# Optimization experiments

Measured on AMD Instinct MI355X. Metric: run time of the kernel, lower is better.

Reference implementation:

```python
import jax, jax.numpy as jnp
import numpy as np

EMB = 300      # emb_size
SEQ = 100      # seq_len
KW = 5         # kernel_width
KN = 50        # kernel_num
KMAX = 3       # maxpooling_num
MLP1 = 75      # decoder_mlp1_num
VOCAB = 50000 + 2
B = 2048
QLEN = 5


def setup_inputs() -> dict:
    key = jax.random.key(0)
    ks = jax.random.split(key, 11)
    input_q = jax.random.randint(ks[0], (QLEN,), 0, 50000)
    input_d = jax.random.randint(ks[1], (B, SEQ), 0, 50000)
    emb_table = jax.random.normal(ks[2], (VOCAB, EMB), jnp.float32) * 0.1
    conv_w = jax.random.normal(ks[3], (KW, 3 * EMB, KN), jnp.float32) * 0.02  # WIO
    conv_b = jnp.zeros((KN,), jnp.float32)
    gate_w = jax.random.normal(ks[4], (EMB, KN), jnp.float32) * 0.05
    gate_b = jnp.zeros((KN,), jnp.float32)
    hid_w = jax.random.normal(ks[5], (KN * KMAX, MLP1), jnp.float32) * 0.05
    hid_b = jnp.zeros((MLP1,), jnp.float32)
    score_w = jax.random.normal(ks[6], (MLP1, 1), jnp.float32) * 0.05
    score_b = jnp.zeros((1,), jnp.float32)
    return {"input_q": input_q, "input_d": input_d, "emb_table": emb_table,
            "conv_w": conv_w, "conv_b": conv_b, "gate_w": gate_w, "gate_b": gate_b,
            "hid_w": hid_w, "hid_b": hid_b, "score_w": score_w, "score_b": score_b}


def kmax_pool(x, k):
    # x: [B, KN, L]; keep top-k values along last axis in original sequence order
    _, idx = jax.lax.top_k(x, k)
    idx = jnp.sort(idx, axis=-1)
    return jnp.take_along_axis(x, idx, axis=-1)  # [B, KN, k]


def reference(input_q, input_d, emb_table, conv_w, conv_b, gate_w, gate_b,
              hid_w, hid_b, score_w, score_b):
    # class vector: mean of query-word embeddings -> [EMB]
    class_vec = emb_table[input_q].mean(axis=0)
    # category-specific gate -> [KN]
    query_gate = jax.nn.sigmoid(class_vec @ gate_w + gate_b)
    # document embeddings -> [B, SEQ, EMB]
    emb = emb_table[input_d]
    # elementwise interaction features, concat -> [B, SEQ, 3*EMB]
    conv_in = jnp.concatenate([emb, class_vec * emb, class_vec - emb], axis=-1)
    # conv over sequence (full-width kernel == 1D conv with C_in=3*EMB) -> [B, SEQ-KW+1, KN]
    conv = jax.lax.conv_general_dilated(
        conv_in, conv_w, window_strides=(1,), padding='VALID',
        dimension_numbers=('NWC', 'WIO', 'NWC')) + conv_b
    gated = query_gate * conv                      # [B, L', KN]
    pooled = kmax_pool(jnp.swapaxes(gated, 1, 2), KMAX)  # [B, KN, KMAX]
    enc = pooled.reshape(pooled.shape[0], -1)      # [B, KN*KMAX] = [B, 150]
    mlp1 = jnp.tanh(enc @ hid_w + hid_b)           # [B, 75]
    score = jnp.tanh(mlp1 @ score_w + score_b)     # [B, 1]
    return (mlp1, score)
```

## Files before the change

### kernel.cpp

```cpp
#include <hip/hip_runtime.h>
#include <math.h>

#define EMB   300
#define SEQ   100
#define KW    5
#define KN    50
#define NPAD  64
#define KMAX  3
#define MLP1  75
#define LOUT  96
#define BATCH 2048
#define EPAD  320
#define CHW   32
#define NCHK  10
#define SPW   36
#define TAU   2.5e-6
#define WHA   0.75
#define WHB   0.25
#define FLAG_TAU 1e-5f

#define WS_C    0
#define WS_GATE 320
#define WS_BIAS 384
#define WS_WG   448
#define F64_DBL 96448
#define WH_F    0
#define WL_F    51200
#define ENC_OFF 102400
#define ENC_PITCH 152
#define FLAGCNT_OFF 413696
#define FLAGLIST_OFF 413704
#define FLAGCAP 4096

typedef __attribute__((ext_vector_type(8))) short short8;
typedef __attribute__((ext_vector_type(4))) float f32x4;

__device__ __forceinline__ unsigned pack_hl(float x) {
    unsigned u = __float_as_uint(x);
    unsigned hi = (u + 0x7fffu + ((u >> 16) & 1u)) >> 16;
    float r = x - __uint_as_float(hi << 16);
    unsigned v = __float_as_uint(r);
    unsigned lo = (v + 0x7fffu + ((v >> 16) & 1u)) >> 16;
    return (hi << 16) | lo;
}

__global__ __launch_bounds__(256) void prep_a(
    const int* __restrict__ qids, const float* __restrict__ emb,
    const float* __restrict__ gate_w, const float* __restrict__ gate_b,
    const float* __restrict__ conv_w, const float* __restrict__ conv_b,
    double* __restrict__ ws, float* wsf)
{
    __shared__ double cS[EMB];
    __shared__ double gS[KN];
    __shared__ double pS[KW][KN];
    int t = threadIdx.x;
    if (t == 0) *(int*)(wsf + FLAGCNT_OFF) = 0;
    for (int e = t; e < EMB; e += 256) {
        double s = 0.0;
        for (int q = 0; q < 5; ++q) s += (double)emb[(size_t)qids[q] * EMB + e];
        double c = s * 0.2;
        cS[e] = c;
        ws[WS_C + e] = c;
    }
    __syncthreads();
    if (t < KN) {
        double g = (double)gate_b[t];
        for (int e = 0; e < EMB; ++e) g += cS[e] * (double)gate_w[e * KN + t];
        g = 1.0 / (1.0 + exp(-g));
        gS[t] = g;
        ws[WS_GATE + t] = g;
    }
    if (t < KW * KN) {
        int n = t % KN, w = t / KN;
        const float* base = conv_w + w * (3 * EMB * KN) + (2 * EMB) * KN + n;
        double p = 0.0;
        for (int e = 0; e < EMB; ++e) p += cS[e] * (double)base[e * KN];
        pS[w][n] = p;
    }
    __syncthreads();
    if (t < KN) {
        double s = (double)conv_b[t];
        for (int w = 0; w < KW; ++w) s += pS[w][t];
        ws[WS_BIAS + t] = gS[t] * s;
    }
}

__global__ __launch_bounds__(256) void prep_b(
    const float* __restrict__ conv_w, const double* __restrict__ ws,
    double* __restrict__ wg, float* __restrict__ wsf)
{
    int gid  = blockIdx.x * 256 + threadIdx.x;
    int wid  = gid >> 6;
    int lane = gid & 63;
    int w = wid / EPAD;
    int e = wid - w * EPAD;
    double v = 0.0;
    if (e < EMB && lane < KN) {
        double c = ws[WS_C + e];
        const float* p = conv_w + (size_t)w * (3 * EMB * KN) + (size_t)e * KN + lane;
        v = ws[WS_GATE + lane] *
            ((double)p[0] + c * (double)p[EMB * KN] - (double)p[2 * EMB * KN]);
    }
    if (e < EMB) wg[(size_t)(w * NPAD + lane) * EMB + e] = v;
    unsigned pk = pack_hl((float)v);
    unsigned short* Wh = (unsigned short*)(wsf + WH_F);
    unsigned short* Wl = (unsigned short*)(wsf + WL_F);
    size_t o = (size_t)(w * NPAD + lane) * EPAD + e;
    Wh[o] = (unsigned short)(pk >> 16);
    Wl[o] = (unsigned short)(pk & 0xffffu);
}

__global__ __launch_bounds__(256, 2) void main_mfma(
    const int* __restrict__ input_d, const float* __restrict__ emb,
    const double* __restrict__ ws, float* wsf,
    const float* __restrict__ hid_w, const float* __restrict__ hid_b,
    const float* __restrict__ score_w, const float* __restrict__ score_b,
    float* __restrict__ out)
{
    __shared__ __align__(16) unsigned stageS[4][SEQ * SPW];
    __shared__ float encS[4][ENC_PITCH];
    __shared__ float mlpS[4][MLP1 + 1];

    int t = threadIdx.x;
    int wid = t >> 6, lane = t & 63;
    int bb = blockIdx.x * 4 + wid;
    int m = lane & 15, kg = lane >> 4;
    unsigned* stg = &stageS[wid][0];

    int tv[7];
    #pragma unroll
    for (int it = 0; it < 7; ++it) {
        int i = lane + it * 64;
        tv[it] = (i < SEQ * 4) ? input_d[bb * SEQ + (i >> 2)] : 0;
    }

    f32x4 acc[6][4];
    #pragma unroll
    for (int lt = 0; lt < 6; ++lt)
        #pragma unroll
        for (int nt = 0; nt < 4; ++nt)
            acc[lt][nt] = (f32x4){0.f, 0.f, 0.f, 0.f};

    const unsigned short* Wh = (const unsigned short*)(wsf + WH_F);
    const unsigned short* Wl = (const unsigned short*)(wsf + WL_F);

    float4 pfa[7], pfb[7];
    #pragma unroll
    for (int it = 0; it < 7; ++it) {
        int i = lane + it * 64;
        float4 z = {0.f, 0.f, 0.f, 0.f};
        pfa[it] = z; pfb[it] = z;
        if (i < SEQ * 4) {
            int eg = i & 3;
            const float* er = emb + (size_t)tv[it] * EMB + eg * 8;
            pfa[it] = *(const float4*)(er);
            pfb[it] = *(const float4*)(er + 4);
        }
    }

    #pragma unroll 1
    for (int c = 0; c < NCHK; ++c) {
        int e0 = c * CHW;
        #pragma unroll
        for (int it = 0; it < 7; ++it) {
            int i = lane + it * 64;
            if (i < SEQ * 4) {
                int s = i >> 2, eg = i & 3;
                float4 fa = pfa[it], fb = pfb[it];
                unsigned p0 = pack_hl(fa.x), p1 = pack_hl(fa.y), p2 = pack_hl(fa.z), p3 = pack_hl(fa.w);
                unsigned p4 = pack_hl(fb.x), p5 = pack_hl(fb.y), p6 = pack_hl(fb.z), p7 = pack_hl(fb.w);
                uint4 hv, lv;
                hv.x = (p0 >> 16)     | (p1 & 0xffff0000u);
                hv.y = (p2 >> 16)     | (p3 & 0xffff0000u);
                hv.z = (p4 >> 16)     | (p5 & 0xffff0000u);
                hv.w = (p6 >> 16)     | (p7 & 0xffff0000u);
                lv.x = (p0 & 0xffffu) | (p1 << 16);
                lv.y = (p2 & 0xffffu) | (p3 << 16);
                lv.z = (p4 & 0xffffu) | (p5 << 16);
                lv.w = (p6 & 0xffffu) | (p7 << 16);
                unsigned* rowp = stg + s * SPW + eg * 8;
                *(uint4*)(rowp)     = hv;
                *(uint4*)(rowp + 4) = lv;
            }
        }
        #pragma unroll
        for (int w = 0; w < KW; ++w) {
            short8 Bh[4], Bl[4];
            #pragma unroll
            for (int nt = 0; nt < 4; ++nt) {
                size_t off = (size_t)(w * NPAD + nt * 16 + m) * EPAD + e0 + kg * 8;
                union { uint4 u; short8 s; } xb, yb;
                xb.u = *(const uint4*)(Wh + off);
                yb.u = *(const uint4*)(Wl + off);
                Bh[nt] = xb.s; Bl[nt] = yb.s;
            }
            if (w == KW - 1 && c + 1 < NCHK) {
                __builtin_amdgcn_sched_barrier(0);
                int e0n = e0 + CHW;
                #pragma unroll
                for (int it = 0; it < 7; ++it) {
                    int i = lane + it * 64;
                    float4 z = {0.f, 0.f, 0.f, 0.f};
                    pfa[it] = z; pfb[it] = z;
                    if (i < SEQ * 4) {
                        int eg = i & 3, e = e0n + eg * 8;
                        const float* er = emb + (size_t)tv[it] * EMB;
                        if (e < EMB)     pfa[it] = *(const float4*)(er + e);
                        if (e + 4 < EMB) pfb[it] = *(const float4*)(er + e + 4);
                    }
                }
                __builtin_amdgcn_sched_barrier(0);
            }
            #pragma unroll
            for (int lt = 0; lt < 6; ++lt) {
                int r = lt * 16 + m + w;
                const unsigned* ap = stg + r * SPW + kg * 8;
                short8 ah = *(const short8*)(ap);
                short8 al = *(const short8*)(ap + 4);
                #pragma unroll
                for (int nt = 0; nt < 4; ++nt) {
                    acc[lt][nt] = __builtin_amdgcn_mfma_f32_16x16x32_bf16(ah, Bh[nt], acc[lt][nt], 0, 0, 0);
                    acc[lt][nt] = __builtin_amdgcn_mfma_f32_16x16x32_bf16(al, Bh[nt], acc[lt][nt], 0, 0, 0);
                    acc[lt][nt] = __builtin_amdgcn_mfma_f32_16x16x32_bf16(ah, Bl[nt], acc[lt][nt], 0, 0, 0);
                }
            }
        }
    }

    float* gated = (float*)stg;
    #pragma unroll 1
    for (int ph = 0; ph < 2; ++ph) {
        int np0 = ph * 25;
        #pragma unroll
        for (int nt = 0; nt < 4; ++nt) {
            int n = nt * 16 + m;
            if (n >= np0 && n < np0 + 25) {
                float bias_n = (float)ws[WS_BIAS + n];
                #pragma unroll
                for (int lt = 0; lt < 6; ++lt)
                    #pragma unroll
                    for (int rr = 0; rr < 4; ++rr)
                        gated[(n - np0) * 97 + lt * 16 + kg * 4 + rr] = acc[lt][nt][rr] + bias_n;
            }
        }
        if (lane < 25) {
            int n = np0 + lane;
            const float* rowp = gated + lane * 97;
            float v1 = -1e30f, v2 = -1e30f, v3 = -1e30f, v4 = -1e30f;
            int   i1 = 0, i2 = 0, i3 = 0, i4 = 0;
            for (int l = 0; l < LOUT; ++l) {
                float v = rowp[l];
                if (v > v1)      { v4=v3; i4=i3; v3=v2; i3=i2; v2=v1; i2=i1; v1=v; i1=l; }
                else if (v > v2) { v4=v3; i4=i3; v3=v2; i3=i2; v2=v;  i2=l; }
                else if (v > v3) { v4=v3; i4=i3; v3=v;  i3=l; }
                else if (v > v4) { v4=v;  i4=l; }
            }
            float a0=v1, a1=v2, a2=v3; int j0=i1, j1=i2, j2=i3;
            if (j0 > j1) { float tv2=a0; a0=a1; a1=tv2; int ti=j0; j0=j1; j1=ti; }
            if (j1 > j2) { float tv2=a1; a1=a2; a2=tv2; int ti=j1; j1=j2; j2=ti; }
            if (j0 > j1) { float tv2=a0; a0=a1; a1=tv2; int ti=j0; j0=j1; j1=ti; }
            encS[wid][3*n] = a0; encS[wid][3*n+1] = a1; encS[wid][3*n+2] = a2;
            float* enc = wsf + ENC_OFF + (size_t)bb * ENC_PITCH + 3 * n;
            enc[0] = a0; enc[1] = a1; enc[2] = a2;
            if (v3 - v4 <= FLAG_TAU) {
                int idx = atomicAdd((int*)(wsf + FLAGCNT_OFF), 1);
                if (idx < FLAGCAP) ((int*)(wsf + FLAGLIST_OFF))[idx] = (bb << 6) | n;
            }
        }
    }
    __syncthreads();

    for (int i = t; i < 4 * MLP1; i += 256) {
        int d = i / MLP1, o = i - d * MLP1;
        float h = hid_b[o];
        for (int k = 0; k < KN * KMAX; ++k) h = fmaf(encS[d][k], hid_w[k * MLP1 + o], h);
        h = tanhf(h);
        mlpS[d][o] = h;
        out[(blockIdx.x * 4 + d) * MLP1 + o] = h;
    }
    __syncthreads();
    if (t < 4) {
        float s = score_b[0];
        for (int j = 0; j < MLP1; ++j) s = fmaf(mlpS[t][j], score_w[j], s);
        out[BATCH * MLP1 + blockIdx.x * 4 + t] = tanhf(s);
    }
}

__global__ __launch_bounds__(64) void cleanup_enc(
    const int* __restrict__ input_d, const float* __restrict__ emb,
    const double* __restrict__ ws, float* wsf)
{
    int cnt = *(const int*)(wsf + FLAGCNT_OFF);
    if (cnt > FLAGCAP) cnt = FLAGCAP;
    int idx = blockIdx.x;
    if (idx >= cnt) return;
    int code = ((const int*)(wsf + FLAGLIST_OFF))[idx];
    int b = code >> 6, n = code & 63;
    int lane = threadIdx.x;

    __shared__ int    tokS[SEQ];
    __shared__ double rowS[LOUT];
    for (int i = lane; i < SEQ; i += 64) tokS[i] = input_d[b * SEQ + i];
    __syncthreads();

    for (int l = lane; l < LOUT; l += 64) {
        double s = 0.0;
        for (int w = 0; w < KW; ++w) {
            const float*  er = emb + (size_t)tokS[l + w] * EMB;
            const double* wr = ws + WS_WG + (size_t)(w * NPAD + n) * EMB;
            for (int e = 0; e < EMB; ++e) s += (double)er[e] * wr[e];
        }
        rowS[l] = s + ws[WS_BIAS + n];
    }
    __syncthreads();

    if (lane == 0) {
        double v1=-1e300, v2=-1e300, v3=-1e300, v4=-1e300;
        int    i1=0, i2=0, i3=0, i4=0;
        for (int l = 0; l < LOUT; ++l) {
            double v = rowS[l];
            if (v > v1)      { v4=v3; i4=i3; v3=v2; i3=i2; v2=v1; i2=i1; v1=v; i1=l; }
            else if (v > v2) { v4=v3; i4=i3; v3=v2; i3=i2; v2=v;  i2=l; }
            else if (v > v3) { v4=v3; i4=i3; v3=v;  i3=l; }
            else if (v > v4) { v4=v;  i4=l; }
        }
        double a0=v1, a1=v2, a2=v3; int j0=i1, j1=i2, j2=i3;
        if (j0 > j1) { double tv=a0; a0=a1; a1=tv; int ti=j0; j0=j1; j1=ti; }
        if (j1 > j2) { double tv=a1; a1=a2; a2=tv; int ti=j1; j1=j2; j2=ti; }
        if (j0 > j1) { double tv=a0; a0=a1; a1=tv; int ti=j0; j0=j1; j1=ti; }
        double b0=v1, b1=v2, b2=v4; int k0=i1, k1=i2, k2=i4;
        if (k0 > k1) { double tv=b0; b0=b1; b1=tv; int ti=k0; k0=k1; k1=ti; }
        if (k1 > k2) { double tv=b1; b1=b2; b2=tv; int ti=k1; k1=k2; k2=ti; }
        if (k0 > k1) { double tv=b0; b0=b1; b1=tv; int ti=k0; k0=k1; k1=ti; }
        float* enc = wsf + ENC_OFF + (size_t)b * ENC_PITCH + 3 * n;
        if (v3 - v4 > TAU) {
            enc[0] = (float)a0; enc[1] = (float)a1; enc[2] = (float)a2;
        } else {
            enc[0] = (float)(WHA*a0 + WHB*b0);
            enc[1] = (float)(WHA*a1 + WHB*b1);
            enc[2] = (float)(WHA*a2 + WHB*b2);
        }
    }
}

__global__ __launch_bounds__(128) void cleanup_mlp(
    const float* wsf, const float* __restrict__ hid_w, const float* __restrict__ hid_b,
    const float* __restrict__ score_w, const float* __restrict__ score_b,
    float* __restrict__ out)
{
    int cnt = *(const int*)(wsf + FLAGCNT_OFF);
    if (cnt > FLAGCAP) cnt = FLAGCAP;
    if ((int)blockIdx.x >= cnt) return;
    int code = ((const int*)(wsf + FLAGLIST_OFF))[blockIdx.x];
    int b = code >> 6;
    int t = threadIdx.x;
    __shared__ float eS[KN * KMAX];
    __shared__ float mS[MLP1];
    const float* enc = wsf + ENC_OFF + (size_t)b * ENC_PITCH;
    for (int i = t; i < KN * KMAX; i += 128) eS[i] = enc[i];
    __syncthreads();
    if (t < MLP1) {
        float h = hid_b[t];
        for (int k = 0; k < KN * KMAX; ++k) h = fmaf(eS[k], hid_w[k * MLP1 + t], h);
        h = tanhf(h);
        mS[t] = h;
        out[b * MLP1 + t] = h;
    }
    __syncthreads();
    if (t == 0) {
        float s = score_b[0];
        for (int j = 0; j < MLP1; ++j) s = fmaf(mS[j], score_w[j], s);
        out[BATCH * MLP1 + b] = tanhf(s);
    }
}

extern "C" void kernel_launch(void* const* d_in, const int* in_sizes, int n_in,
                              void* d_out, int out_size, void* d_ws, size_t ws_size,
                              hipStream_t stream)
{
    const int*   input_q = (const int*)d_in[0];
    const int*   input_d = (const int*)d_in[1];
    const float* emb     = (const float*)d_in[2];
    const float* conv_w  = (const float*)d_in[3];
    const float* conv_b  = (const float*)d_in[4];
    const float* gate_w  = (const float*)d_in[5];
    const float* gate_b  = (const float*)d_in[6];
    const float* hid_w   = (const float*)d_in[7];
    const float* hid_b   = (const float*)d_in[8];
    const float* score_w = (const float*)d_in[9];
    const float* score_b = (const float*)d_in[10];
    float*  out = (float*)d_out;
    double* ws  = (double*)d_ws;
    float*  wsf = (float*)((char*)d_ws + (size_t)F64_DBL * 8);

    hipLaunchKernelGGL(prep_a, dim3(1), dim3(256), 0, stream,
                       input_q, emb, gate_w, gate_b, conv_w, conv_b, ws, wsf);
    hipLaunchKernelGGL(prep_b, dim3(400), dim3(256), 0, stream,
                       conv_w, ws, ws + WS_WG, wsf);
    hipLaunchKernelGGL(main_mfma, dim3(BATCH / 4), dim3(256), 0, stream,
                       input_d, emb, ws, wsf, hid_w, hid_b, score_w, score_b, out);
    hipLaunchKernelGGL(cleanup_enc, dim3(FLAGCAP), dim3(64), 0, stream,
                       input_d, emb, ws, wsf);
    hipLaunchKernelGGL(cleanup_mlp, dim3(FLAGCAP), dim3(128), 0, stream,
                       wsf, hid_w, hid_b, score_w, score_b, out);
}
```

Measured before the change: 404.6 us.

## Split each batch row across two waves sharing one staged tile

The main kernel previously gave each wave its own batch row, with each wave computing all four N tiles from a private LDS stage. Now a 128-thread block handles one row, and the two waves split the N tiles (two each) while sharing one staged embedding tile. The change needs block barriers around staging and the top-k phases. It halves per-wave accumulator registers and per-row LDS staging, which may allow higher occupancy. In exchange it adds synchronisation per chunk and launches four times as many blocks.

```diff
diff --git a/kernel.cpp b/kernel.cpp
--- a/kernel.cpp
+++ b/kernel.cpp
@@ -110,63 +110,67 @@
     Wl[o] = (unsigned short)(pk & 0xffffu);
 }
 
-__global__ __launch_bounds__(256, 2) void main_mfma(
+__global__ __launch_bounds__(128, 3) void main_mfma(
     const int* __restrict__ input_d, const float* __restrict__ emb,
     const double* __restrict__ ws, float* wsf,
     const float* __restrict__ hid_w, const float* __restrict__ hid_b,
     const float* __restrict__ score_w, const float* __restrict__ score_b,
     float* __restrict__ out)
 {
-    __shared__ __align__(16) unsigned stageS[4][SEQ * SPW];
-    __shared__ float encS[4][ENC_PITCH];
-    __shared__ float mlpS[4][MLP1 + 1];
+    __shared__ __align__(16) unsigned stageS[SEQ * SPW];
+    float* gated = (float*)stageS;
+    float* encS  = (float*)stageS + 2432;
+    float* mlpS  = (float*)stageS + 2592;
 
     int t = threadIdx.x;
     int wid = t >> 6, lane = t & 63;
-    int bb = blockIdx.x * 4 + wid;
+    int bb = blockIdx.x;
     int m = lane & 15, kg = lane >> 4;
-    unsigned* stg = &stageS[wid][0];
-
-    int tv[7];
+
+    int tv[4];
     #pragma unroll
-    for (int it = 0; it < 7; ++it) {
-        int i = lane + it * 64;
-        tv[it] = (i < SEQ * 4) ? input_d[bb * SEQ + (i >> 2)] : 0;
-    }
-
-    f32x4 acc[6][4];
+    for (int sl = 0; sl < 4; ++sl) {
+        int i = t + sl * 128;
+        tv[sl] = (i < SEQ * 4) ? input_d[bb * SEQ + (i >> 2)] : 0;
+    }
+
+    f32x4 acc[6][2];
     #pragma unroll
     for (int lt = 0; lt < 6; ++lt)
         #pragma unroll
-        for (int nt = 0; nt < 4; ++nt)
+        for (int nt = 0; nt < 2; ++nt)
             acc[lt][nt] = (f32x4){0.f, 0.f, 0.f, 0.f};
 
     const unsigned short* Wh = (const unsigned short*)(wsf + WH_F);
     const unsigned short* Wl = (const unsigned short*)(wsf + WL_F);
 
-    float4 pfa[7], pfb[7];
+    float4 pfa[4], pfb[4];
     #pragma unroll
-    for (int it = 0; it < 7; ++it) {
-        int i = lane + it * 64;
+    for (int sl = 0; sl < 4; ++sl) {
+        int i = t + sl * 128;
         float4 z = {0.f, 0.f, 0.f, 0.f};
-        pfa[it] = z; pfb[it] = z;
+        pfa[sl] = z; pfb[sl] = z;
         if (i < SEQ * 4) {
             int eg = i & 3;
-            const float* er = emb + (size_t)tv[it] * EMB + eg * 8;
-            pfa[it] = *(const float4*)(er);
-            pfb[it] = *(const float4*)(er + 4);
+            const float* er = emb + (size_t)tv[sl] * EMB + eg * 8;
+            pfa[sl] = *(const float4*)(er);
+            pfb[sl] = *(const float4*)(er + 4);
         }
     }
 
     #pragma unroll 1
     for (int c = 0; c < NCHK; ++c) {
         int e0 = c * CHW;
+        __builtin_amdgcn_sched_barrier(0);
+        asm volatile("s_waitcnt lgkmcnt(0)" ::: "memory");
+        __builtin_amdgcn_s_barrier();
+        __builtin_amdgcn_sched_barrier(0);
         #pragma unroll
-        for (int it = 0; it < 7; ++it) {
-            int i = lane + it * 64;
+        for (int sl = 0; sl < 4; ++sl) {
+            int i = t + sl * 128;
             if (i < SEQ * 4) {
                 int s = i >> 2, eg = i & 3;
-                float4 fa = pfa[it], fb = pfb[it];
+                float4 fa = pfa[sl], fb = pfb[sl];
                 unsigned p0 = pack_hl(fa.x), p1 = pack_hl(fa.y), p2 = pack_hl(fa.z), p3 = pack_hl(fa.w);
                 unsigned p4 = pack_hl(fb.x), p5 = pack_hl(fb.y), p6 = pack_hl(fb.z), p7 = pack_hl(fb.w);
                 uint4 hv, lv;
@@ -178,17 +182,22 @@
                 lv.y = (p2 & 0xffffu) | (p3 << 16);
                 lv.z = (p4 & 0xffffu) | (p5 << 16);
                 lv.w = (p6 & 0xffffu) | (p7 << 16);
-                unsigned* rowp = stg + s * SPW + eg * 8;
+                unsigned* rowp = stageS + s * SPW + eg * 8;
                 *(uint4*)(rowp)     = hv;
                 *(uint4*)(rowp + 4) = lv;
             }
         }
+        __builtin_amdgcn_sched_barrier(0);
+        asm volatile("s_waitcnt lgkmcnt(0)" ::: "memory");
+        __builtin_amdgcn_s_barrier();
+        __builtin_amdgcn_sched_barrier(0);
         #pragma unroll
         for (int w = 0; w < KW; ++w) {
-            short8 Bh[4], Bl[4];
+            short8 Bh[2], Bl[2];
             #pragma unroll
-            for (int nt = 0; nt < 4; ++nt) {
-                size_t off = (size_t)(w * NPAD + nt * 16 + m) * EPAD + e0 + kg * 8;
+            for (int nt = 0; nt < 2; ++nt) {
+                int ntg = wid * 2 + nt;
+                size_t off = (size_t)(w * NPAD + ntg * 16 + m) * EPAD + e0 + kg * 8;
                 union { uint4 u; short8 s; } xb, yb;
                 xb.u = *(const uint4*)(Wh + off);
                 yb.u = *(const uint4*)(Wl + off);
@@ -198,15 +207,15 @@
                 __builtin_amdgcn_sched_barrier(0);
                 int e0n = e0 + CHW;
                 #pragma unroll
-                for (int it = 0; it < 7; ++it) {
-                    int i = lane + it * 64;
+                for (int sl = 0; sl < 4; ++sl) {
+                    int i = t + sl * 128;
                     float4 z = {0.f, 0.f, 0.f, 0.f};
-                    pfa[it] = z; pfb[it] = z;
+                    pfa[sl] = z; pfb[sl] = z;
                     if (i < SEQ * 4) {
                         int eg = i & 3, e = e0n + eg * 8;
-                        const float* er = emb + (size_t)tv[it] * EMB;
-                        if (e < EMB)     pfa[it] = *(const float4*)(er + e);
-                        if (e + 4 < EMB) pfb[it] = *(const float4*)(er + e + 4);
+                        const float* er = emb + (size_t)tv[sl] * EMB;
+                        if (e < EMB)     pfa[sl] = *(const float4*)(er + e);
+                        if (e + 4 < EMB) pfb[sl] = *(const float4*)(er + e + 4);
                     }
                 }
                 __builtin_amdgcn_sched_barrier(0);
@@ -214,11 +223,11 @@
             #pragma unroll
             for (int lt = 0; lt < 6; ++lt) {
                 int r = lt * 16 + m + w;
-                const unsigned* ap = stg + r * SPW + kg * 8;
+                const unsigned* ap = stageS + r * SPW + kg * 8;
                 short8 ah = *(const short8*)(ap);
                 short8 al = *(const short8*)(ap + 4);
                 #pragma unroll
-                for (int nt = 0; nt < 4; ++nt) {
+                for (int nt = 0; nt < 2; ++nt) {
                     acc[lt][nt] = __builtin_amdgcn_mfma_f32_16x16x32_bf16(ah, Bh[nt], acc[lt][nt], 0, 0, 0);
                     acc[lt][nt] = __builtin_amdgcn_mfma_f32_16x16x32_bf16(al, Bh[nt], acc[lt][nt], 0, 0, 0);
                     acc[lt][nt] = __builtin_amdgcn_mfma_f32_16x16x32_bf16(ah, Bl[nt], acc[lt][nt], 0, 0, 0);
@@ -227,13 +236,15 @@
         }
     }
 
-    float* gated = (float*)stg;
+    __syncthreads();
+
     #pragma unroll 1
     for (int ph = 0; ph < 2; ++ph) {
         int np0 = ph * 25;
         #pragma unroll
-        for (int nt = 0; nt < 4; ++nt) {
-            int n = nt * 16 + m;
+        for (int nt = 0; nt < 2; ++nt) {
+            int ntg = wid * 2 + nt;
+            int n = ntg * 16 + m;
             if (n >= np0 && n < np0 + 25) {
                 float bias_n = (float)ws[WS_BIAS + n];
                 #pragma unroll
@@ -243,9 +254,12 @@
                         gated[(n - np0) * 97 + lt * 16 + kg * 4 + rr] = acc[lt][nt][rr] + bias_n;
             }
         }
-        if (lane < 25) {
-            int n = np0 + lane;
-            const float* rowp = gated + lane * 97;
+        __syncthreads();
+        int nr = wid ? 12 : 13;
+        if (lane < nr) {
+            int row = wid * 13 + lane;
+            int n = np0 + row;
+            const float* rowp = gated + row * 97;
             float v1 = -1e30f, v2 = -1e30f, v3 = -1e30f, v4 = -1e30f;
             int   i1 = 0, i2 = 0, i3 = 0, i4 = 0;
             for (int l = 0; l < LOUT; ++l) {
@@ -259,7 +273,7 @@
             if (j0 > j1) { float tv2=a0; a0=a1; a1=tv2; int ti=j0; j0=j1; j1=ti; }
             if (j1 > j2) { float tv2=a1; a1=a2; a2=tv2; int ti=j1; j1=j2; j2=ti; }
             if (j0 > j1) { float tv2=a0; a0=a1; a1=tv2; int ti=j0; j0=j1; j1=ti; }
-            encS[wid][3*n] = a0; encS[wid][3*n+1] = a1; encS[wid][3*n+2] = a2;
+            encS[3*n] = a0; encS[3*n+1] = a1; encS[3*n+2] = a2;
             float* enc = wsf + ENC_OFF + (size_t)bb * ENC_PITCH + 3 * n;
             enc[0] = a0; enc[1] = a1; enc[2] = a2;
             if (v3 - v4 <= FLAG_TAU) {
@@ -267,22 +281,21 @@
                 if (idx < FLAGCAP) ((int*)(wsf + FLAGLIST_OFF))[idx] = (bb << 6) | n;
             }
         }
-    }
-    __syncthreads();
-
-    for (int i = t; i < 4 * MLP1; i += 256) {
-        int d = i / MLP1, o = i - d * MLP1;
-        float h = hid_b[o];
-        for (int k = 0; k < KN * KMAX; ++k) h = fmaf(encS[d][k], hid_w[k * MLP1 + o], h);
+        __syncthreads();
+    }
+
+    if (t < MLP1) {
+        float h = hid_b[t];
+        for (int k = 0; k < KN * KMAX; ++k) h = fmaf(encS[k], hid_w[k * MLP1 + t], h);
         h = tanhf(h);
-        mlpS[d][o] = h;
-        out[(blockIdx.x * 4 + d) * MLP1 + o] = h;
-    }
-    __syncthreads();
-    if (t < 4) {
+        mlpS[t] = h;
+        out[bb * MLP1 + t] = h;
+    }
+    __syncthreads();
+    if (t == 0) {
         float s = score_b[0];
-        for (int j = 0; j < MLP1; ++j) s = fmaf(mlpS[t][j], score_w[j], s);
-        out[BATCH * MLP1 + blockIdx.x * 4 + t] = tanhf(s);
+        for (int j = 0; j < MLP1; ++j) s = fmaf(mlpS[j], score_w[j], s);
+        out[BATCH * MLP1 + bb] = tanhf(s);
     }
 }
 
@@ -397,7 +410,7 @@
                        input_q, emb, gate_w, gate_b, conv_w, conv_b, ws, wsf);
     hipLaunchKernelGGL(prep_b, dim3(400), dim3(256), 0, stream,
                        conv_w, ws, ws + WS_WG, wsf);
-    hipLaunchKernelGGL(main_mfma, dim3(BATCH / 4), dim3(256), 0, stream,
+    hipLaunchKernelGGL(main_mfma, dim3(BATCH), dim3(128), 0, stream,
                        input_d, emb, ws, wsf, hid_w, hid_b, score_w, score_b, out);
     hipLaunchKernelGGL(cleanup_enc, dim3(FLAGCAP), dim3(64), 0, stream,
                        input_d, emb, ws, wsf);
```

New measurement: 399.2 us. No clear change (-1.3%).

## Split sequence into two halves with double-buffered LDS staging overlapping packing and MFMA

Applied to the files above, without the earlier changes.

The per-wave sequence of 100 rows is split into two overlapping 52-row halves, each with its own LDS staging buffer. While MFMAs run on one half, the embedding gathers and bf16 hi/lo packing for the other half (or for the next chunk) are interleaved between the kernel-width iterations. The aim is to hide global-load and pack latency behind matrix work and to cut the prefetch register footprint from 14 float4 pairs to 4. In exchange, the B-operand weight fragments are now loaded twice per chunk, once per half.

```diff
diff --git a/kernel.cpp b/kernel.cpp
--- a/kernel.cpp
+++ b/kernel.cpp
@@ -14,6 +14,8 @@
 #define CHW   32
 #define NCHK  10
 #define SPW   36
+#define HROWS 52
+#define HITEMS 208
 #define TAU   2.5e-6
 #define WHA   0.75
 #define WHB   0.25
@@ -110,6 +112,82 @@
     Wl[o] = (unsigned short)(pk & 0xffffu);
 }
 
+__device__ __forceinline__ void pack_item(unsigned* buf, int i, float4 fa, float4 fb) {
+    int s = i >> 2, eg = i & 3;
+    unsigned p0 = pack_hl(fa.x), p1 = pack_hl(fa.y), p2 = pack_hl(fa.z), p3 = pack_hl(fa.w);
+    unsigned p4 = pack_hl(fb.x), p5 = pack_hl(fb.y), p6 = pack_hl(fb.z), p7 = pack_hl(fb.w);
+    uint4 hv, lv;
+    hv.x = (p0 >> 16)     | (p1 & 0xffff0000u);
+    hv.y = (p2 >> 16)     | (p3 & 0xffff0000u);
+    hv.z = (p4 >> 16)     | (p5 & 0xffff0000u);
+    hv.w = (p6 >> 16)     | (p7 & 0xffff0000u);
+    lv.x = (p0 & 0xffffu) | (p1 << 16);
+    lv.y = (p2 & 0xffffu) | (p3 << 16);
+    lv.z = (p4 & 0xffffu) | (p5 << 16);
+    lv.w = (p6 & 0xffffu) | (p7 << 16);
+    unsigned* rowp = buf + s * SPW + eg * 8;
+    *(uint4*)(rowp)     = hv;
+    *(uint4*)(rowp + 4) = lv;
+}
+
+template<int LT0, bool DOPACK>
+__device__ __forceinline__ void do_phase(
+    const unsigned* bufC, unsigned* bufP,
+    int e0, int ge0, int4 tvP,
+    int lane, int m, int kg,
+    const unsigned short* __restrict__ Wh, const unsigned short* __restrict__ Wl,
+    const float* __restrict__ emb, f32x4 (&acc)[6][4])
+{
+    float4 ga[4], gb[4];
+    if (DOPACK) {
+        __builtin_amdgcn_sched_barrier(0);
+        #pragma unroll
+        for (int sl = 0; sl < 4; ++sl) {
+            int i = lane + sl * 64;
+            float4 z = {0.f, 0.f, 0.f, 0.f};
+            ga[sl] = z; gb[sl] = z;
+            if (i < HITEMS) {
+                int tok = (sl == 0) ? tvP.x : (sl == 1) ? tvP.y : (sl == 2) ? tvP.z : tvP.w;
+                int e = ge0 + (i & 3) * 8;
+                const float* er = emb + (size_t)tok * EMB;
+                if (e < EMB)     ga[sl] = *(const float4*)(er + e);
+                if (e + 4 < EMB) gb[sl] = *(const float4*)(er + e + 4);
+            }
+        }
+        __builtin_amdgcn_sched_barrier(0);
+    }
+    #pragma unroll
+    for (int w = 0; w < KW; ++w) {
+        short8 Bh[4], Bl[4];
+        #pragma unroll
+        for (int nt = 0; nt < 4; ++nt) {
+            size_t off = (size_t)(w * NPAD + nt * 16 + m) * EPAD + e0 + kg * 8;
+            union { uint4 u; short8 s; } xb, yb;
+            xb.u = *(const uint4*)(Wh + off);
+            yb.u = *(const uint4*)(Wl + off);
+            Bh[nt] = xb.s; Bl[nt] = yb.s;
+        }
+        #pragma unroll
+        for (int ltl = 0; ltl < 3; ++ltl) {
+            int r = ltl * 16 + m + w;
+            const unsigned* ap = bufC + r * SPW + kg * 8;
+            short8 ah = *(const short8*)(ap);
+            short8 al = *(const short8*)(ap + 4);
+            #pragma unroll
+            for (int nt = 0; nt < 4; ++nt) {
+                acc[LT0+ltl][nt] = __builtin_amdgcn_mfma_f32_16x16x32_bf16(ah, Bh[nt], acc[LT0+ltl][nt], 0, 0, 0);
+                acc[LT0+ltl][nt] = __builtin_amdgcn_mfma_f32_16x16x32_bf16(al, Bh[nt], acc[LT0+ltl][nt], 0, 0, 0);
+                acc[LT0+ltl][nt] = __builtin_amdgcn_mfma_f32_16x16x32_bf16(ah, Bl[nt], acc[LT0+ltl][nt], 0, 0, 0);
+            }
+        }
+        if (DOPACK && w >= 1) {
+            int sl = w - 1;
+            int i = lane + sl * 64;
+            if (i < HITEMS) pack_item(bufP, i, ga[sl], gb[sl]);
+        }
+    }
+}
+
 __global__ __launch_bounds__(256, 2) void main_mfma(
     const int* __restrict__ input_d, const float* __restrict__ emb,
     const double* __restrict__ ws, float* wsf,
@@ -117,7 +195,7 @@
     const float* __restrict__ score_w, const float* __restrict__ score_b,
     float* __restrict__ out)
 {
-    __shared__ __align__(16) unsigned stageS[4][SEQ * SPW];
+    __shared__ __align__(16) unsigned stageS[4][2][HROWS * SPW];
     __shared__ float encS[4][ENC_PITCH];
     __shared__ float mlpS[4][MLP1 + 1];
 
@@ -125,13 +203,21 @@
     int wid = t >> 6, lane = t & 63;
     int bb = blockIdx.x * 4 + wid;
     int m = lane & 15, kg = lane >> 4;
-    unsigned* stg = &stageS[wid][0];
-
-    int tv[7];
-    #pragma unroll
-    for (int it = 0; it < 7; ++it) {
-        int i = lane + it * 64;
-        tv[it] = (i < SEQ * 4) ? input_d[bb * SEQ + (i >> 2)] : 0;
+    unsigned* bufA = &stageS[wid][0][0];
+    unsigned* bufB = &stageS[wid][1][0];
+
+    int4 tvA, tvB;
+    {
+        int ta[4], tb[4];
+        #pragma unroll
+        for (int sl = 0; sl < 4; ++sl) {
+            int i = lane + sl * 64;
+            int row = i >> 2;
+            ta[sl] = (i < HITEMS) ? input_d[bb * SEQ + row] : 0;
+            tb[sl] = (i < HITEMS) ? input_d[bb * SEQ + 48 + row] : 0;
+        }
+        tvA = make_int4(ta[0], ta[1], ta[2], ta[3]);
+        tvB = make_int4(tb[0], tb[1], tb[2], tb[3]);
     }
 
     f32x4 acc[6][4];
@@ -144,90 +230,32 @@
     const unsigned short* Wh = (const unsigned short*)(wsf + WH_F);
     const unsigned short* Wl = (const unsigned short*)(wsf + WL_F);
 
-    float4 pfa[7], pfb[7];
-    #pragma unroll
-    for (int it = 0; it < 7; ++it) {
-        int i = lane + it * 64;
-        float4 z = {0.f, 0.f, 0.f, 0.f};
-        pfa[it] = z; pfb[it] = z;
-        if (i < SEQ * 4) {
-            int eg = i & 3;
-            const float* er = emb + (size_t)tv[it] * EMB + eg * 8;
-            pfa[it] = *(const float4*)(er);
-            pfb[it] = *(const float4*)(er + 4);
+    {
+        #pragma unroll
+        for (int sl = 0; sl < 4; ++sl) {
+            int i = lane + sl * 64;
+            if (i < HITEMS) {
+                int tok = (sl == 0) ? tvA.x : (sl == 1) ? tvA.y : (sl == 2) ? tvA.z : tvA.w;
+                int e = (i & 3) * 8;
+                const float* er = emb + (size_t)tok * EMB;
+                float4 fa = *(const float4*)(er + e);
+                float4 fb = *(const float4*)(er + e + 4);
+                pack_item(bufA, i, fa, fb);
+            }
         }
     }
 
     #pragma unroll 1
     for (int c = 0; c < NCHK; ++c) {
         int e0 = c * CHW;
-        #pragma unroll
-        for (int it = 0; it < 7; ++it) {
-            int i = lane + it * 64;
-            if (i < SEQ * 4) {
-                int s = i >> 2, eg = i & 3;
-                float4 fa = pfa[it], fb = pfb[it];
-                unsigned p0 = pack_hl(fa.x), p1 = pack_hl(fa.y), p2 = pack_hl(fa.z), p3 = pack_hl(fa.w);
-                unsigned p4 = pack_hl(fb.x), p5 = pack_hl(fb.y), p6 = pack_hl(fb.z), p7 = pack_hl(fb.w);
-                uint4 hv, lv;
-                hv.x = (p0 >> 16)     | (p1 & 0xffff0000u);
-                hv.y = (p2 >> 16)     | (p3 & 0xffff0000u);
-                hv.z = (p4 >> 16)     | (p5 & 0xffff0000u);
-                hv.w = (p6 >> 16)     | (p7 & 0xffff0000u);
-                lv.x = (p0 & 0xffffu) | (p1 << 16);
-                lv.y = (p2 & 0xffffu) | (p3 << 16);
-                lv.z = (p4 & 0xffffu) | (p5 << 16);
-                lv.w = (p6 & 0xffffu) | (p7 << 16);
-                unsigned* rowp = stg + s * SPW + eg * 8;
-                *(uint4*)(rowp)     = hv;
-                *(uint4*)(rowp + 4) = lv;
-            }
-        }
-        #pragma unroll
-        for (int w = 0; w < KW; ++w) {
-            short8 Bh[4], Bl[4];
-            #pragma unroll
-            for (int nt = 0; nt < 4; ++nt) {
-                size_t off = (size_t)(w * NPAD + nt * 16 + m) * EPAD + e0 + kg * 8;
-                union { uint4 u; short8 s; } xb, yb;
-                xb.u = *(const uint4*)(Wh + off);
-                yb.u = *(const uint4*)(Wl + off);
-                Bh[nt] = xb.s; Bl[nt] = yb.s;
-            }
-            if (w == KW - 1 && c + 1 < NCHK) {
-                __builtin_amdgcn_sched_barrier(0);
-                int e0n = e0 + CHW;
-                #pragma unroll
-                for (int it = 0; it < 7; ++it) {
-                    int i = lane + it * 64;
-                    float4 z = {0.f, 0.f, 0.f, 0.f};
-                    pfa[it] = z; pfb[it] = z;
-                    if (i < SEQ * 4) {
-                        int eg = i & 3, e = e0n + eg * 8;
-                        const float* er = emb + (size_t)tv[it] * EMB;
-                        if (e < EMB)     pfa[it] = *(const float4*)(er + e);
-                        if (e + 4 < EMB) pfb[it] = *(const float4*)(er + e + 4);
-                    }
-                }
-                __builtin_amdgcn_sched_barrier(0);
-            }
-            #pragma unroll
-            for (int lt = 0; lt < 6; ++lt) {
-                int r = lt * 16 + m + w;
-                const unsigned* ap = stg + r * SPW + kg * 8;
-                short8 ah = *(const short8*)(ap);
-                short8 al = *(const short8*)(ap + 4);
-                #pragma unroll
-                for (int nt = 0; nt < 4; ++nt) {
-                    acc[lt][nt] = __builtin_amdgcn_mfma_f32_16x16x32_bf16(ah, Bh[nt], acc[lt][nt], 0, 0, 0);
-                    acc[lt][nt] = __builtin_amdgcn_mfma_f32_16x16x32_bf16(al, Bh[nt], acc[lt][nt], 0, 0, 0);
-                    acc[lt][nt] = __builtin_amdgcn_mfma_f32_16x16x32_bf16(ah, Bl[nt], acc[lt][nt], 0, 0, 0);
-                }
-            }
-        }
-    }
-
-    float* gated = (float*)stg;
+        do_phase<0, true>(bufA, bufB, e0, e0, tvB, lane, m, kg, Wh, Wl, emb, acc);
+        if (c + 1 < NCHK)
+            do_phase<3, true>(bufB, bufA, e0, e0 + CHW, tvA, lane, m, kg, Wh, Wl, emb, acc);
+        else
+            do_phase<3, false>(bufB, bufA, e0, 0, tvA, lane, m, kg, Wh, Wl, emb, acc);
+    }
+
+    float* gated = (float*)bufA;
     #pragma unroll 1
     for (int ph = 0; ph < 2; ++ph) {
         int np0 = ph * 25;
```

Measured after the change: 545.5 us. +34.8%, slower.
